# Kernel optimization log

Measured on AMD Instinct MI355X. Metric: run time of the kernel, lower is better.

The kernel has to match this reference:

```python
import jax, jax.numpy as jnp
import numpy as np

NH = 12        # main attention heads (head_dim = 64)
SNH = 4        # scorer self-attention heads
ALPHA = 0.1    # static survival-score weight
EPS = 1e-8


def _linear(x, w, b):
    # torch nn.Linear: y = x @ W^T + b
    return x @ w.T + b


def _mha(x, in_w, in_b, out_w, out_b, n_heads, maskf):
    # torch nn.MultiheadAttention (batch_first, eval mode)
    B, S, D = x.shape
    hd = D // n_heads
    qkv = _linear(x, in_w, in_b)                      # [B,S,3D]
    q, k, v = jnp.split(qkv, 3, axis=-1)
    sp = lambda t: t.reshape(B, S, n_heads, hd).transpose(0, 2, 1, 3)
    q, k, v = sp(q), sp(k), sp(v)                     # [B,h,S,hd]
    scores = jnp.einsum('bhqd,bhkd->bhqk', q, k) / jnp.asarray(np.sqrt(hd), x.dtype)
    scores = jnp.where(maskf[:, None, None, :] > 0, scores, jnp.asarray(-1e9, x.dtype))
    aw = jax.nn.softmax(scores, axis=-1)
    o = jnp.einsum('bhqk,bhkd->bhqd', aw, v).transpose(0, 2, 1, 3).reshape(B, S, D)
    return _linear(o, out_w, out_b)


def _survival_scores(x, maskf, sp_w, sp_b, sa_in_w, sa_in_b, sa_out_w, sa_out_b,
                     nw1, nb1, nw2, nb2, mw1, mb1, mw2, mb2, dw1, db1, dw2, db2):
    h = _linear(x, sp_w, sp_b)                        # [B,S,256]
    h = _mha(h, sa_in_w, sa_in_b, sa_out_w, sa_out_b, SNH, maskf)
    n = jax.nn.softplus(_linear(jax.nn.relu(_linear(h, nw1, nb1)), nw2, nb2))[..., 0]
    mu = jax.nn.sigmoid(_linear(jax.nn.relu(_linear(h, mw1, mb1)), mw2, mb2))[..., 0]
    delta = jax.nn.relu(_linear(jax.nn.relu(_linear(h, dw1, db1)), dw2, db2))[..., 0]
    # S = log(N) + log(mu / mu_c) - delta, with mu_c = 1.0
    return jnp.log(n + EPS) + jnp.log(mu + EPS) - delta


def setup_inputs() -> dict:
    key = jax.random.key(0)
    ks = iter(jax.random.split(key, 40))
    W = lambda shape: jax.random.normal(next(ks), shape, jnp.float32) * 0.05
    Z = lambda shape: jnp.zeros(shape, jnp.float32)
    B, S, H, I = 2, 2048, 768, 256
    inp = {
        'x': jax.random.normal(next(ks), (B, S, H), jnp.float32),
        'mask': jnp.ones((B, S), jnp.int32),
        'qw': W((H, H)), 'qb': Z((H,)),
        'kw': W((H, H)), 'kb': Z((H,)),
        'vw': W((H, H)), 'vb': Z((H,)),
        'ow': W((H, H)), 'ob': Z((H,)),
        'sp_w': W((I, H)), 'sp_b': Z((I,)),
        'sa_in_w': W((3 * I, I)), 'sa_in_b': Z((3 * I,)),
        'sa_out_w': W((I, I)), 'sa_out_b': Z((I,)),
        'nw1': W((I // 2, I)), 'nb1': Z((I // 2,)), 'nw2': W((1, I // 2)), 'nb2': Z((1,)),
        'mw1': W((I // 2, I)), 'mb1': Z((I // 2,)), 'mw2': W((1, I // 2)), 'mb2': Z((1,)),
        'dw1': W((I // 2, I)), 'db1': Z((I // 2,)), 'dw2': W((1, I // 2)), 'db2': Z((1,)),
    }
    return inp


def reference(x, mask, qw, qb, kw, kb, vw, vb, ow, ob,
              sp_w, sp_b, sa_in_w, sa_in_b, sa_out_w, sa_out_b,
              nw1, nb1, nw2, nb2, mw1, mb1, mw2, mb2, dw1, db1, dw2, db2):
    B, S, H = x.shape
    hd = H // NH
    maskf = mask.astype(x.dtype)
    # Q/K/V projections -> [B,h,S,hd]
    sp = lambda t: t.reshape(B, S, NH, hd).transpose(0, 2, 1, 3)
    q = sp(_linear(x, qw, qb))
    k = sp(_linear(x, kw, kb))
    v = sp(_linear(x, vw, vb))
    scores = jnp.einsum('bhqd,bhkd->bhqk', q, k) / jnp.asarray(np.sqrt(hd), x.dtype)
    # survival-score bias (broadcast over heads and query positions)
    surv = _survival_scores(x, maskf, sp_w, sp_b, sa_in_w, sa_in_b, sa_out_w, sa_out_b,
                            nw1, nb1, nw2, nb2, mw1, mb1, mw2, mb2, dw1, db1, dw2, db2)
    scores = scores + ALPHA * surv[:, None, None, :]
    scores = scores + (1.0 - maskf)[:, None, None, :] * -1e9
    aw = jax.nn.softmax(scores, axis=-1)
    out = jnp.einsum('bhqk,bhkd->bhqd', aw, v).transpose(0, 2, 1, 3).reshape(B, S, H)
    return _linear(out, ow, ob)
```

## Files before the change

### kernel.cpp

```cpp
#include <hip/hip_runtime.h>
#include <math.h>

typedef __bf16 bf16;
typedef __bf16 bfrag __attribute__((ext_vector_type(8)));
typedef __bf16 bf4 __attribute__((ext_vector_type(4)));
typedef float f4 __attribute__((ext_vector_type(4)));
typedef float f16v __attribute__((ext_vector_type(16)));

#define LOG2E 1.4426950408889634f

#define DEV static __device__ __forceinline__

DEV f4 MFMA(bfrag a, bfrag b, f4 c) {
  return __builtin_amdgcn_mfma_f32_16x16x32_bf16(a, b, c, 0, 0, 0);
}
DEV f16v MFMA32(bfrag a, bfrag b, f16v c) {
  return __builtin_amdgcn_mfma_f32_32x32x16_bf16(a, b, c, 0, 0, 0);
}
DEV float ex2(float x) { return __builtin_amdgcn_exp2f(x); }
DEV unsigned pkbf(float a, float b) {
  bf16 ha = (bf16)a, hb = (bf16)b;
  unsigned short ua = __builtin_bit_cast(unsigned short, ha);
  unsigned short ub = __builtin_bit_cast(unsigned short, hb);
  return (unsigned)ua | ((unsigned)ub << 16);
}
DEV void gload_lds16(const bf16* g, bf16* l) {
  __builtin_amdgcn_global_load_lds(
      (const __attribute__((address_space(1))) void*)g,
      (__attribute__((address_space(3))) void*)l, 16, 0, 0);
}

__global__ __launch_bounds__(256) void pack_all(
    const float* __restrict__ x, const float* __restrict__ qw, const float* __restrict__ kw,
    const float* __restrict__ vw, const float* __restrict__ ow, const float* __restrict__ sp_w,
    const float* __restrict__ sa_in_w, const float* __restrict__ sa_out_w,
    const float* __restrict__ nw1, const float* __restrict__ mw1, const float* __restrict__ dw1,
    const float* __restrict__ qb, const float* __restrict__ kb, const float* __restrict__ vb,
    const float* __restrict__ nb1, const float* __restrict__ mb1, const float* __restrict__ db1,
    const int* __restrict__ mask,
    bf16* __restrict__ xb, bf16* __restrict__ wqkv, bf16* __restrict__ wob,
    bf16* __restrict__ spwb, bf16* __restrict__ sainb, bf16* __restrict__ saoutb,
    bf16* __restrict__ w1pack, float* __restrict__ bqkv, float* __restrict__ b1pack,
    float* __restrict__ maskBias) {
  int bid = blockIdx.x;
  int tid = threadIdx.x;
  const float* src = nullptr;
  bf16* dst = nullptr;
  int rel = 0;
  if (bid < 3072)      { src = x;       dst = xb;                   rel = bid; }
  else if (bid < 3648) { src = qw;      dst = wqkv;                 rel = bid - 3072; }
  else if (bid < 4224) { src = kw;      dst = wqkv + 589824;        rel = bid - 3648; }
  else if (bid < 4800) { src = vw;      dst = wqkv + 2 * 589824;    rel = bid - 4224; }
  else if (bid < 5376) { src = ow;      dst = wob;                  rel = bid - 4800; }
  else if (bid < 5568) { src = sp_w;    dst = spwb;                 rel = bid - 5376; }
  else if (bid < 5760) { src = sa_in_w; dst = sainb;                rel = bid - 5568; }
  else if (bid < 5824) { src = sa_out_w;dst = saoutb;               rel = bid - 5760; }
  else if (bid < 5856) { src = nw1;     dst = w1pack;               rel = bid - 5824; }
  else if (bid < 5888) { src = mw1;     dst = w1pack + 32768;       rel = bid - 5856; }
  else if (bid < 5920) { src = dw1;     dst = w1pack + 2 * 32768;   rel = bid - 5888; }
  else if (bid == 5920) {
    if (tid < 576) {
      int which = tid / 192, j = tid % 192;
      const float* s = which == 0 ? qb : (which == 1 ? kb : vb);
      reinterpret_cast<float4*>(bqkv)[tid] = reinterpret_cast<const float4*>(s)[j];
    }
    return;
  } else if (bid == 5921) {
    if (tid < 96) {
      int which = tid / 32, j = tid % 32;
      const float* s = which == 0 ? nb1 : (which == 1 ? mb1 : db1);
      reinterpret_cast<float4*>(b1pack)[tid] = reinterpret_cast<const float4*>(s)[j];
    }
    return;
  } else {
    int idx = (bid - 5922) * 256 + tid;
    int4 m = reinterpret_cast<const int4*>(mask)[idx];
    float4 o;
    o.x = m.x > 0 ? 0.f : -1e9f * LOG2E;
    o.y = m.y > 0 ? 0.f : -1e9f * LOG2E;
    o.z = m.z > 0 ? 0.f : -1e9f * LOG2E;
    o.w = m.w > 0 ? 0.f : -1e9f * LOG2E;
    reinterpret_cast<float4*>(maskBias)[idx] = o;
    return;
  }
  int i = rel * 256 + tid;
  float4 v = reinterpret_cast<const float4*>(src)[i];
  bf4 o;
  o[0] = (bf16)v.x; o[1] = (bf16)v.y; o[2] = (bf16)v.z; o[3] = (bf16)v.w;
  reinterpret_cast<bf4*>(dst)[i] = o;
}

template<int OUTF32, int RELU>
__global__ __launch_bounds__(256) void gemm_nt(
    const bf16* __restrict__ A, int lda,
    const bf16* __restrict__ W, int ldw,
    const float* __restrict__ bias,
    void* __restrict__ C, int ldc,
    int N64, int K) {
  int lane = threadIdx.x & 63;
  int w = threadIdx.x >> 6;
  int lrow = lane & 15, lgrp = lane >> 4;
  int tn = blockIdx.x % N64, tm = blockIdx.x / N64;
  int m0 = tm * 64 + (w >> 1) * 32;
  int n0 = tn * 64 + (w & 1) * 32;
  const bf16* Ab = A + (size_t)m0 * lda + lgrp * 8;
  const bf16* Wb = W + (size_t)n0 * ldw + lgrp * 8;
  f4 acc[2][2] = {};
  for (int k0 = 0; k0 < K; k0 += 32) {
    bfrag a0 = *(const bfrag*)(Ab + (size_t)lrow * lda + k0);
    bfrag a1 = *(const bfrag*)(Ab + (size_t)(lrow + 16) * lda + k0);
    bfrag b0 = *(const bfrag*)(Wb + (size_t)lrow * ldw + k0);
    bfrag b1 = *(const bfrag*)(Wb + (size_t)(lrow + 16) * ldw + k0);
    acc[0][0] = MFMA(a0, b0, acc[0][0]);
    acc[0][1] = MFMA(a0, b1, acc[0][1]);
    acc[1][0] = MFMA(a1, b0, acc[1][0]);
    acc[1][1] = MFMA(a1, b1, acc[1][1]);
  }
#pragma unroll
  for (int mi = 0; mi < 2; mi++)
#pragma unroll
    for (int nj = 0; nj < 2; nj++) {
      int col = n0 + nj * 16 + lrow;
      float bv = bias[col];
      int rowb = m0 + mi * 16 + lgrp * 4;
#pragma unroll
      for (int i = 0; i < 4; i++) {
        float v = acc[mi][nj][i] + bv;
        if (RELU) v = fmaxf(v, 0.f);
        if (OUTF32)
          ((float*)C)[(size_t)(rowb + i) * ldc + col] = v;
        else
          ((bf16*)C)[(size_t)(rowb + i) * ldc + col] = (bf16)v;
      }
    }
}

template<int OUTF32>
__global__ __launch_bounds__(256, 2) void gemm_big(
    const bf16* __restrict__ A,
    const bf16* __restrict__ W,
    const float* __restrict__ bias,
    void* __restrict__ C, int ldc,
    int N128, int K) {
  __shared__ char smem[65536];
  int lane = threadIdx.x & 63;
  int w = threadIdx.x >> 6;
  int lrow = lane & 15, lgrp = lane >> 4;
  int tn = blockIdx.x % N128, tm = blockIdx.x / N128;
  int m0 = tm * 128, n0 = tn * 128;

  int srow = lane >> 3;
  int sslot = (lane & 7) ^ srow;

  auto stage = [&](int bufb, int k0) {
#pragma unroll
    for (int j = 0; j < 4; j++) {
      int rb = (w * 4 + j) * 8 + srow;
      gload_lds16(A + (size_t)(m0 + rb) * K + k0 + sslot * 8,
                  (bf16*)(smem + bufb + (w * 4 + j) * 1024));
      gload_lds16(W + (size_t)(n0 + rb) * K + k0 + sslot * 8,
                  (bf16*)(smem + bufb + 16384 + (w * 4 + j) * 1024));
    }
  };

  f4 acc[4][4] = {};
  int swz = (lrow & 7) << 4;
  int mbase = (w >> 1) * 64, nbase = (w & 1) * 64;

  stage(0, 0);
  __syncthreads();
  int buf = 0;
  int nt = K / 64;
  for (int t = 0; t < nt; t++) {
    int nbuf = buf ^ 32768;
    if (t + 1 < nt) stage(nbuf, (t + 1) * 64);
    const char* As = smem + buf;
    const char* Ws = smem + buf + 16384;
#pragma unroll
    for (int kb = 0; kb < 128; kb += 64) {
      bfrag a[4], b[4];
#pragma unroll
      for (int i = 0; i < 4; i++) {
        a[i] = *(const bfrag*)(As + (mbase + i * 16 + lrow) * 128 + ((kb + lgrp * 16) ^ swz));
        b[i] = *(const bfrag*)(Ws + (nbase + i * 16 + lrow) * 128 + ((kb + lgrp * 16) ^ swz));
      }
#pragma unroll
      for (int mi = 0; mi < 4; mi++)
#pragma unroll
        for (int nj = 0; nj < 4; nj++)
          acc[mi][nj] = MFMA(a[mi], b[nj], acc[mi][nj]);
    }
    __syncthreads();
    buf = nbuf;
  }

#pragma unroll
  for (int mi = 0; mi < 4; mi++)
#pragma unroll
    for (int nj = 0; nj < 4; nj++) {
      int col = n0 + nbase + nj * 16 + lrow;
      float bv = bias[col];
      int rowb = m0 + mbase + mi * 16 + lgrp * 4;
#pragma unroll
      for (int i = 0; i < 4; i++) {
        float v = acc[mi][nj][i] + bv;
        if (OUTF32)
          ((float*)C)[(size_t)(rowb + i) * ldc + col] = v;
        else
          ((bf16*)C)[(size_t)(rowb + i) * ldc + col] = (bf16)v;
      }
    }
}

__global__ __launch_bounds__(256) void vtrans(const bf16* __restrict__ V, int rs, int coff,
                                              bf16* __restrict__ Vt, int H, int S) {
  int nst = S / 64;
  int st = blockIdx.x % nst;
  int h = (blockIdx.x / nst) % H;
  int b = blockIdx.x / (nst * H);
  __shared__ bf16 tile[64][72];
  int t = threadIdx.x;
  int r = t >> 2, c = t & 3;
  const bf16* src = V + ((size_t)b * S + st * 64 + r) * rs + coff + h * 64 + c * 16;
  bfrag v0 = *(const bfrag*)(src);
  bfrag v1 = *(const bfrag*)(src + 8);
  *(bfrag*)&tile[r][c * 16] = v0;
  *(bfrag*)&tile[r][c * 16 + 8] = v1;
  __syncthreads();
  bf16* dst = Vt + (((size_t)b * H + h) * 64 + r) * S + st * 64 + c * 16;
  bfrag o0, o1;
#pragma unroll
  for (int j = 0; j < 8; j++) {
    o0[j] = tile[c * 16 + j][r];
    o1[j] = tile[c * 16 + 8 + j][r];
  }
  *(bfrag*)dst = o0;
  *(bfrag*)(dst + 8) = o1;
}

template<int SPLIT, int PARTIAL>
__global__ __launch_bounds__(256) void flash7_k(
    const bf16* __restrict__ Q, const bf16* __restrict__ Kp, int rs,
    const bf16* __restrict__ Vt, const float* __restrict__ bias,
    bf16* __restrict__ O, int ors,
    float* __restrict__ Opart, float* __restrict__ Lpart,
    int H, int S, float scale, int Bc) {
  int nqt = S / 128;
  int bid = blockIdx.x;
  int qt = bid % nqt;
  int hh = (bid / nqt) % H;
  int b = (bid / (nqt * H)) % Bc;
  int sp = bid / (nqt * H * Bc);
  int lane = threadIdx.x & 63, w = threadIdx.x >> 6;
  int l31 = lane & 31, hf = lane >> 5;
  int q0 = qt * 128 + w * 32;
  const int kchunk = S / SPLIT;
  int k_beg = sp * kchunk;
  int swzl = (l31 & 7) << 4;

  const bf16* Qb = Q + ((size_t)b * S + q0 + l31) * rs + hh * 64 + hf * 8;
  bfrag qf[4];
#pragma unroll
  for (int c = 0; c < 4; c++) qf[c] = *(const bfrag*)(Qb + 16 * c);

  const bf16* gK0 = Kp + ((size_t)b * S + k_beg) * rs + hh * 64;
  const bf16* gV0 = Vt + (((size_t)b * H + hh) * 64) * (size_t)S + k_beg;
  const float* biasb = bias + (size_t)b * S;

  __shared__ bf16 KT[2][4096];
  __shared__ bf16 VT[2][4096];

  f16v acc0, acc1;
#pragma unroll
  for (int r = 0; r < 16; r++) { acc0[r] = 0.f; acc1[r] = 0.f; }
  float lrun = 0.f;

  int srow = lane >> 3;
  int sel = ((lane & 7) ^ srow) * 8;
  int r0 = (w * 2) * 8 + srow;
  int r1 = (w * 2 + 1) * 8 + srow;

  auto stage = [&](int bb, int kt) {
    const bf16* gK = gK0 + (size_t)(kt - k_beg) * rs;
    const bf16* gV = gV0 + (kt - k_beg);
    gload_lds16(gK + (size_t)r0 * rs + sel, KT[bb] + (w * 2) * 512);
    gload_lds16(gK + (size_t)r1 * rs + sel, KT[bb] + (w * 2 + 1) * 512);
    gload_lds16(gV + (size_t)r0 * S + sel, VT[bb] + (w * 2) * 512);
    gload_lds16(gV + (size_t)r1 * S + sel, VT[bb] + (w * 2 + 1) * 512);
  };

  stage(0, k_beg);
  __syncthreads();

  const int nt = kchunk / 64;
  int buf = 0;
  for (int t = 0; t < nt; t++) {
    int kt = k_beg + t * 64;
    if (t + 1 < nt) stage(buf ^ 1, kt + 64);

    const char* KTb = (const char*)KT[buf];
    const char* VTb = (const char*)VT[buf];

    f16v s_lo, s_hi;
#pragma unroll
    for (int r = 0; r < 16; r++) { s_lo[r] = 0.f; s_hi[r] = 0.f; }
#pragma unroll
    for (int c = 0; c < 4; c++) {
      int colb = 32 * c + 16 * hf;
      bfrag klo = *(const bfrag*)(KTb + l31 * 128 + (colb ^ swzl));
      bfrag khi = *(const bfrag*)(KTb + (32 + l31) * 128 + (colb ^ swzl));
      s_lo = MFMA32(klo, qf[c], s_lo);
      s_hi = MFMA32(khi, qf[c], s_hi);
    }

    f4 blo[4], bhi[4];
#pragma unroll
    for (int g = 0; g < 4; g++) {
      blo[g] = *(const f4*)(biasb + kt + g * 8 + hf * 4);
      bhi[g] = *(const f4*)(biasb + kt + 32 + g * 8 + hf * 4);
    }
#pragma unroll
    for (int r = 0; r < 16; r++) {
      s_lo[r] = ex2(s_lo[r] * scale + blo[r >> 2][r & 3]);
      s_hi[r] = ex2(s_hi[r] * scale + bhi[r >> 2][r & 3]);
    }
    float rsum = s_lo[0] + s_hi[0];
#pragma unroll
    for (int r = 1; r < 16; r++) rsum += s_lo[r] + s_hi[r];
    rsum += __shfl_xor(rsum, 32);
    lrun += rsum;

    bfrag pb[4];
#pragma unroll
    for (int cc = 0; cc < 4; cc++) {
      const f16v& sv = (cc < 2) ? s_lo : s_hi;
      int rb = (cc & 1) * 8;
      unsigned lo0 = pkbf(sv[rb + 0], sv[rb + 1]);
      unsigned lo1 = pkbf(sv[rb + 2], sv[rb + 3]);
      unsigned hi0 = pkbf(sv[rb + 4], sv[rb + 5]);
      unsigned hi1 = pkbf(sv[rb + 6], sv[rb + 7]);
      unsigned t0 = hf ? lo0 : hi0;
      unsigned t1 = hf ? lo1 : hi1;
      unsigned r0s = (unsigned)__shfl_xor((int)t0, 32);
      unsigned r1s = (unsigned)__shfl_xor((int)t1, 32);
      union { bfrag v; unsigned u[4]; } pu;
      pu.u[0] = hf ? r0s : lo0;
      pu.u[1] = hf ? r1s : lo1;
      pu.u[2] = hf ? hi0 : r0s;
      pu.u[3] = hf ? hi1 : r1s;
      pb[cc] = pu.v;
    }

#pragma unroll
    for (int c = 0; c < 4; c++) {
      int colb = 32 * c + 16 * hf;
      bfrag v0 = *(const bfrag*)(VTb + l31 * 128 + (colb ^ swzl));
      bfrag v1 = *(const bfrag*)(VTb + (32 + l31) * 128 + (colb ^ swzl));
      acc0 = MFMA32(v0, pb[c], acc0);
      acc1 = MFMA32(v1, pb[c], acc1);
    }

    __syncthreads();
    buf ^= 1;
  }

  int q = q0 + l31;
  if (PARTIAL) {
    float* op = Opart + ((((size_t)sp * Bc + b) * H + hh) * S + q) * 64 + hf * 4;
#pragma unroll
    for (int g = 0; g < 4; g++) {
      f4 v0, v1;
#pragma unroll
      for (int i = 0; i < 4; i++) { v0[i] = acc0[4 * g + i]; v1[i] = acc1[4 * g + i]; }
      *(f4*)(op + g * 8) = v0;
      *(f4*)(op + 32 + g * 8) = v1;
    }
    if (hf == 0)
      Lpart[(((size_t)sp * Bc + b) * H + hh) * S + q] = lrun;
  } else {
    float inv = 1.f / lrun;
    bf16* Ob = O + ((size_t)b * S + q) * ors + hh * 64 + hf * 4;
#pragma unroll
    for (int g = 0; g < 4; g++) {
      bf4 o0, o1;
#pragma unroll
      for (int i = 0; i < 4; i++) {
        o0[i] = (bf16)(acc0[4 * g + i] * inv);
        o1[i] = (bf16)(acc1[4 * g + i] * inv);
      }
      *(bf4*)(Ob + g * 8) = o0;
      *(bf4*)(Ob + 32 + g * 8) = o1;
    }
  }
}

__global__ __launch_bounds__(256) void flash_comb(
    const float* __restrict__ Opart, const float* __restrict__ L,
    bf16* __restrict__ O, int ors, int Hh, int S, int Bc, int nsplit) {
  int idx = blockIdx.x * 256 + threadIdx.x;
  int d4 = idx & 15;
  int q = (idx >> 4) % S;
  int hh = ((idx >> 4) / S) % Hh;
  int b = (idx >> 4) / (S * Hh);
  size_t rowstride = (size_t)Bc * Hh * S;
  size_t rbase = ((size_t)b * Hh + hh) * S + q;
  float lsum = 0.f;
  f4 o = {0.f, 0.f, 0.f, 0.f};
  for (int sp = 0; sp < nsplit; sp++) {
    lsum += L[sp * rowstride + rbase];
    f4 a = *(const f4*)(Opart + (sp * rowstride + rbase) * 64 + d4 * 4);
#pragma unroll
    for (int i = 0; i < 4; i++) o[i] += a[i];
  }
  float inv = 1.f / lsum;
  bf4 obv;
#pragma unroll
  for (int i = 0; i < 4; i++) obv[i] = (bf16)(o[i] * inv);
  *(bf4*)(O + ((size_t)b * S + q) * ors + hh * 64 + d4 * 4) = obv;
}

__global__ __launch_bounds__(256) void surv_k(
    const bf16* __restrict__ hid,
    const float* __restrict__ nw2, const float* __restrict__ nb2,
    const float* __restrict__ mw2, const float* __restrict__ mb2,
    const float* __restrict__ dw2, const float* __restrict__ db2,
    const float* __restrict__ maskBias, float* __restrict__ biasMain) {
  int w = threadIdx.x >> 6, lane = threadIdx.x & 63;
  int row = blockIdx.x * 4 + w;
  const bf16* hr = hid + (size_t)row * 384;
  const float* W2[3] = {nw2, mw2, dw2};
  float outs[3];
#pragma unroll
  for (int t = 0; t < 3; t++) {
    float acc = (float)hr[t * 128 + lane] * W2[t][lane] +
                (float)hr[t * 128 + 64 + lane] * W2[t][64 + lane];
    for (int msk = 1; msk < 64; msk <<= 1) acc += __shfl_xor(acc, msk);
    outs[t] = acc;
  }
  if (lane == 0) {
    float xn = outs[0] + nb2[0];
    float n = (xn > 20.f) ? xn : log1pf(__expf(xn));
    float mu = 1.f / (1.f + __expf(-(outs[1] + mb2[0])));
    float delta = fmaxf(outs[2] + db2[0], 0.f);
    float surv = logf(n + 1e-8f) + logf(mu + 1e-8f) - delta;
    biasMain[row] = 0.1f * LOG2E * surv + maskBias[row];
  }
}

extern "C" void kernel_launch(void* const* d_in, const int* in_sizes, int n_in,
                              void* d_out, int out_size, void* d_ws, size_t ws_size,
                              hipStream_t stream) {
  const int B = 2, S = 2048, H = 768, I = 256;
  const int NH = 12, SNH = 4;
  const int M = B * S;
  const float SC = 0.125f * LOG2E;

  const float* x = (const float*)d_in[0];
  const int* mask = (const int*)d_in[1];
  const float* qw = (const float*)d_in[2];
  const float* qb = (const float*)d_in[3];
  const float* kw = (const float*)d_in[4];
  const float* kb = (const float*)d_in[5];
  const float* vw = (const float*)d_in[6];
  const float* vb = (const float*)d_in[7];
  const float* ow = (const float*)d_in[8];
  const float* ob = (const float*)d_in[9];
  const float* sp_w = (const float*)d_in[10];
  const float* sp_b = (const float*)d_in[11];
  const float* sa_in_w = (const float*)d_in[12];
  const float* sa_in_b = (const float*)d_in[13];
  const float* sa_out_w = (const float*)d_in[14];
  const float* sa_out_b = (const float*)d_in[15];
  const float* nw1 = (const float*)d_in[16];
  const float* nb1 = (const float*)d_in[17];
  const float* nw2 = (const float*)d_in[18];
  const float* nb2 = (const float*)d_in[19];
  const float* mw1 = (const float*)d_in[20];
  const float* mb1 = (const float*)d_in[21];
  const float* mw2 = (const float*)d_in[22];
  const float* mb2 = (const float*)d_in[23];
  const float* dw1 = (const float*)d_in[24];
  const float* db1 = (const float*)d_in[25];
  const float* dw2 = (const float*)d_in[26];
  const float* db2 = (const float*)d_in[27];

  char* ws = (char*)d_ws;
  size_t off = 0;
  auto alloc = [&](size_t bytes) -> void* {
    void* p = ws + off;
    off += (bytes + 255) & ~(size_t)255;
    return p;
  };

  bf16* xb = (bf16*)alloc((size_t)M * H * 2);
  bf16* wqkv = (bf16*)alloc((size_t)3 * H * H * 2);
  float* bqkv = (float*)alloc((size_t)3 * H * 4);
  bf16* wob = (bf16*)alloc((size_t)H * H * 2);
  bf16* spwb = (bf16*)alloc((size_t)I * H * 2);
  bf16* sainb = (bf16*)alloc((size_t)(3 * I) * I * 2);
  bf16* saoutb = (bf16*)alloc((size_t)I * I * 2);
  bf16* w1pack = (bf16*)alloc((size_t)384 * 256 * 2);
  float* b1pack = (float*)alloc((size_t)384 * 4);
  float* maskBias = (float*)alloc((size_t)M * 4);
  float* biasMain = (float*)alloc((size_t)M * 4);

  const int SPM = 2, SPS = 4;
  size_t offMark = off;
  bf16* h0 = (bf16*)alloc((size_t)M * I * 2);
  bf16* qkv_s = (bf16*)alloc((size_t)M * (3 * I) * 2);
  bf16* vt_s = (bf16*)alloc((size_t)B * SNH * 64 * S * 2);
  bf16* attn_s = (bf16*)alloc((size_t)M * I * 2);
  bf16* h1 = (bf16*)alloc((size_t)M * I * 2);
  bf16* hid = (bf16*)alloc((size_t)M * 384 * 2);
  float* Opart_s = (float*)alloc((size_t)SPS * B * SNH * S * 64 * 4);
  float* L_s = (float*)alloc((size_t)SPS * B * SNH * S * 4);
  size_t endA = off;
  off = offMark;
  bf16* QKVm = (bf16*)alloc((size_t)M * 3 * H * 2);
  bf16* vt_m = (bf16*)alloc((size_t)B * NH * 64 * S * 2);
  bf16* attn_m = (bf16*)alloc((size_t)M * H * 2);
  float* Opart_m = (float*)alloc((size_t)SPM * B * NH * S * 64 * 4);
  float* L_m = (float*)alloc((size_t)SPM * B * NH * S * 4);
  size_t endB = off;
  size_t need = endA > endB ? endA : endB;
  bool split_ok = ws_size >= need;
  (void)in_sizes; (void)n_in; (void)out_size;

  pack_all<<<5926, 256, 0, stream>>>(x, qw, kw, vw, ow, sp_w, sa_in_w, sa_out_w, nw1, mw1, dw1,
                                     qb, kb, vb, nb1, mb1, db1, mask,
                                     xb, wqkv, wob, spwb, sainb, saoutb, w1pack, bqkv, b1pack,
                                     maskBias);

  gemm_nt<0, 0><<<(M / 64) * (I / 64), 256, 0, stream>>>(xb, H, spwb, H, sp_b, h0, I, I / 64, H);
  gemm_nt<0, 0><<<(M / 64) * ((3 * I) / 64), 256, 0, stream>>>(h0, I, sainb, I, sa_in_b, qkv_s,
                                                               3 * I, (3 * I) / 64, I);
  vtrans<<<B * SNH * (S / 64), 256, 0, stream>>>(qkv_s, 3 * I, 2 * I, vt_s, SNH, S);
  if (split_ok) {
    flash7_k<SPS, 1><<<SPS * B * SNH * (S / 128), 256, 0, stream>>>(
        qkv_s, qkv_s + I, 3 * I, vt_s, maskBias, nullptr, 0, Opart_s, L_s, SNH, S, SC, B);
    flash_comb<<<(B * SNH * S * 16) / 256, 256, 0, stream>>>(Opart_s, L_s, attn_s, I, SNH, S,
                                                             B, SPS);
  } else {
    flash7_k<1, 0><<<B * SNH * (S / 128), 256, 0, stream>>>(
        qkv_s, qkv_s + I, 3 * I, vt_s, maskBias, attn_s, I, nullptr, nullptr, SNH, S, SC, B);
  }
  gemm_nt<0, 0><<<(M / 64) * (I / 64), 256, 0, stream>>>(attn_s, I, saoutb, I, sa_out_b, h1, I,
                                                         I / 64, I);
  gemm_nt<0, 1><<<(M / 64) * (384 / 64), 256, 0, stream>>>(h1, I, w1pack, I, b1pack, hid, 384,
                                                           384 / 64, I);
  surv_k<<<M / 4, 256, 0, stream>>>(hid, nw2, nb2, mw2, mb2, dw2, db2, maskBias, biasMain);

  gemm_big<0><<<(M / 128) * (3 * H / 128), 256, 0, stream>>>(xb, wqkv, bqkv, QKVm, 3 * H,
                                                             3 * H / 128, H);
  vtrans<<<B * NH * (S / 64), 256, 0, stream>>>(QKVm, 3 * H, 2 * H, vt_m, NH, S);
  if (split_ok) {
    flash7_k<SPM, 1><<<SPM * B * NH * (S / 128), 256, 0, stream>>>(
        QKVm, QKVm + H, 3 * H, vt_m, biasMain, nullptr, 0, Opart_m, L_m, NH, S, SC, B);
    flash_comb<<<(B * NH * S * 16) / 256, 256, 0, stream>>>(Opart_m, L_m, attn_m, H, NH, S, B,
                                                            SPM);
  } else {
    flash7_k<1, 0><<<B * NH * (S / 128), 256, 0, stream>>>(
        QKVm, QKVm + H, 3 * H, vt_m, biasMain, attn_m, H, nullptr, nullptr, NH, S, SC, B);
  }
  gemm_big<1><<<(M / 128) * (H / 128), 256, 0, stream>>>(attn_m, wob, ob, d_out, H,
                                                         H / 128, H);
}
```

Measured before the change: 196.8 us.

## Split KV range across warp pairs inside block and merge in LDS

The flash attention kernel now uses 64-query tiles, with the block's two warp pairs each processing half of the KV chunk. Their partial accumulators and row sums are merged through shared memory, which replaces a cross-block split plus combine kernel for the main attention and halves the scorer split. It also uses v_cvt_pk_bf16_f32 and permlane32_swap for the P fragment repack, and adds s_setprio around the MFMA sections. The cost is 64KB of LDS per block, which may limit occupancy, plus an extra barrier and exchange at the end.

After: 197.5 us. About the same (+0.4%).

```diff
diff --git a/kernel.cpp b/kernel.cpp
--- a/kernel.cpp
+++ b/kernel.cpp
@@ -6,6 +6,7 @@
 typedef __bf16 bf4 __attribute__((ext_vector_type(4)));
 typedef float f4 __attribute__((ext_vector_type(4)));
 typedef float f16v __attribute__((ext_vector_type(16)));
+typedef unsigned uint2v __attribute__((ext_vector_type(2)));
 
 #define LOG2E 1.4426950408889634f
 
@@ -18,11 +19,8 @@
   return __builtin_amdgcn_mfma_f32_32x32x16_bf16(a, b, c, 0, 0, 0);
 }
 DEV float ex2(float x) { return __builtin_amdgcn_exp2f(x); }
-DEV unsigned pkbf(float a, float b) {
-  bf16 ha = (bf16)a, hb = (bf16)b;
-  unsigned short ua = __builtin_bit_cast(unsigned short, ha);
-  unsigned short ub = __builtin_bit_cast(unsigned short, hb);
-  return (unsigned)ua | ((unsigned)ub << 16);
+DEV uint2v pl32(unsigned a, unsigned b) {
+  return __builtin_amdgcn_permlane32_swap(a, b, false, false);
 }
 DEV void gload_lds16(const bf16* g, bf16* l) {
   __builtin_amdgcn_global_load_lds(
@@ -239,23 +237,26 @@
 }
 
 template<int SPLIT, int PARTIAL>
-__global__ __launch_bounds__(256) void flash7_k(
+__global__ __launch_bounds__(256) void flash8_k(
     const bf16* __restrict__ Q, const bf16* __restrict__ Kp, int rs,
     const bf16* __restrict__ Vt, const float* __restrict__ bias,
     bf16* __restrict__ O, int ors,
     float* __restrict__ Opart, float* __restrict__ Lpart,
     int H, int S, float scale, int Bc) {
-  int nqt = S / 128;
+  __shared__ char smem[65536];
+  int nqt = S / 64;
   int bid = blockIdx.x;
   int qt = bid % nqt;
   int hh = (bid / nqt) % H;
   int b = (bid / (nqt * H)) % Bc;
   int sp = bid / (nqt * H * Bc);
   int lane = threadIdx.x & 63, w = threadIdx.x >> 6;
+  int wi = w & 1, half = w >> 1;
   int l31 = lane & 31, hf = lane >> 5;
-  int q0 = qt * 128 + w * 32;
+  int q0 = qt * 64 + wi * 32;
   const int kchunk = S / SPLIT;
-  int k_beg = sp * kchunk;
+  const int khalf = kchunk / 2;
+  int k_beg = sp * kchunk + half * khalf;
   int swzl = (l31 & 7) << 4;
 
   const bf16* Qb = Q + ((size_t)b * S + q0 + l31) * rs + hh * 64 + hf * 8;
@@ -267,9 +268,6 @@
   const bf16* gV0 = Vt + (((size_t)b * H + hh) * 64) * (size_t)S + k_beg;
   const float* biasb = bias + (size_t)b * S;
 
-  __shared__ bf16 KT[2][4096];
-  __shared__ bf16 VT[2][4096];
-
   f16v acc0, acc1;
 #pragma unroll
   for (int r = 0; r < 16; r++) { acc0[r] = 0.f; acc1[r] = 0.f; }
@@ -277,33 +275,35 @@
 
   int srow = lane >> 3;
   int sel = ((lane & 7) ^ srow) * 8;
-  int r0 = (w * 2) * 8 + srow;
-  int r1 = (w * 2 + 1) * 8 + srow;
-
-  auto stage = [&](int bb, int kt) {
-    const bf16* gK = gK0 + (size_t)(kt - k_beg) * rs;
-    const bf16* gV = gV0 + (kt - k_beg);
-    gload_lds16(gK + (size_t)r0 * rs + sel, KT[bb] + (w * 2) * 512);
-    gload_lds16(gK + (size_t)r1 * rs + sel, KT[bb] + (w * 2 + 1) * 512);
-    gload_lds16(gV + (size_t)r0 * S + sel, VT[bb] + (w * 2) * 512);
-    gload_lds16(gV + (size_t)r1 * S + sel, VT[bb] + (w * 2 + 1) * 512);
+
+  auto stage = [&](int bb, int trel) {
+    const bf16* gK = gK0 + (size_t)trel * 64 * rs;
+    const bf16* gV = gV0 + trel * 64;
+    char* base = smem + (half * 2 + bb) * 16384;
+#pragma unroll
+    for (int j = 0; j < 4; j++) {
+      int r = wi * 32 + j * 8 + srow;
+      gload_lds16(gK + (size_t)r * rs + sel, (bf16*)(base + (wi * 32 + j * 8) * 128));
+      gload_lds16(gV + (size_t)r * S + sel, (bf16*)(base + 8192 + (wi * 32 + j * 8) * 128));
+    }
   };
 
-  stage(0, k_beg);
+  stage(0, 0);
   __syncthreads();
 
-  const int nt = kchunk / 64;
+  const int nt = khalf / 64;
   int buf = 0;
   for (int t = 0; t < nt; t++) {
     int kt = k_beg + t * 64;
-    if (t + 1 < nt) stage(buf ^ 1, kt + 64);
-
-    const char* KTb = (const char*)KT[buf];
-    const char* VTb = (const char*)VT[buf];
+    if (t + 1 < nt) stage(buf ^ 1, t + 1);
+
+    const char* KTb = smem + (half * 2 + buf) * 16384;
+    const char* VTb = KTb + 8192;
 
     f16v s_lo, s_hi;
 #pragma unroll
     for (int r = 0; r < 16; r++) { s_lo[r] = 0.f; s_hi[r] = 0.f; }
+    __builtin_amdgcn_s_setprio(1);
 #pragma unroll
     for (int c = 0; c < 4; c++) {
       int colb = 32 * c + 16 * hf;
@@ -312,6 +312,7 @@
       s_lo = MFMA32(klo, qf[c], s_lo);
       s_hi = MFMA32(khi, qf[c], s_hi);
     }
+    __builtin_amdgcn_s_setprio(0);
 
     f4 blo[4], bhi[4];
 #pragma unroll
@@ -335,22 +336,19 @@
     for (int cc = 0; cc < 4; cc++) {
       const f16v& sv = (cc < 2) ? s_lo : s_hi;
       int rb = (cc & 1) * 8;
-      unsigned lo0 = pkbf(sv[rb + 0], sv[rb + 1]);
-      unsigned lo1 = pkbf(sv[rb + 2], sv[rb + 3]);
-      unsigned hi0 = pkbf(sv[rb + 4], sv[rb + 5]);
-      unsigned hi1 = pkbf(sv[rb + 6], sv[rb + 7]);
-      unsigned t0 = hf ? lo0 : hi0;
-      unsigned t1 = hf ? lo1 : hi1;
-      unsigned r0s = (unsigned)__shfl_xor((int)t0, 32);
-      unsigned r1s = (unsigned)__shfl_xor((int)t1, 32);
+      unsigned lo0, lo1, hi0, hi1;
+      asm("v_cvt_pk_bf16_f32 %0, %1, %2" : "=v"(lo0) : "v"(sv[rb + 0]), "v"(sv[rb + 1]));
+      asm("v_cvt_pk_bf16_f32 %0, %1, %2" : "=v"(lo1) : "v"(sv[rb + 2]), "v"(sv[rb + 3]));
+      asm("v_cvt_pk_bf16_f32 %0, %1, %2" : "=v"(hi0) : "v"(sv[rb + 4]), "v"(sv[rb + 5]));
+      asm("v_cvt_pk_bf16_f32 %0, %1, %2" : "=v"(hi1) : "v"(sv[rb + 6]), "v"(sv[rb + 7]));
+      uint2v e0 = pl32(lo0, hi0);
+      uint2v e1 = pl32(lo1, hi1);
       union { bfrag v; unsigned u[4]; } pu;
-      pu.u[0] = hf ? r0s : lo0;
-      pu.u[1] = hf ? r1s : lo1;
-      pu.u[2] = hf ? hi0 : r0s;
-      pu.u[3] = hf ? hi1 : r1s;
+      pu.u[0] = e0[0]; pu.u[1] = e1[0]; pu.u[2] = e0[1]; pu.u[3] = e1[1];
       pb[cc] = pu.v;
     }
 
+    __builtin_amdgcn_s_setprio(1);
 #pragma unroll
     for (int c = 0; c < 4; c++) {
       int colb = 32 * c + 16 * hf;
@@ -359,37 +357,64 @@
       acc0 = MFMA32(v0, pb[c], acc0);
       acc1 = MFMA32(v1, pb[c], acc1);
     }
+    __builtin_amdgcn_s_setprio(0);
 
     __syncthreads();
     buf ^= 1;
   }
 
-  int q = q0 + l31;
-  if (PARTIAL) {
-    float* op = Opart + ((((size_t)sp * Bc + b) * H + hh) * S + q) * 64 + hf * 4;
-#pragma unroll
-    for (int g = 0; g < 4; g++) {
-      f4 v0, v1;
-#pragma unroll
-      for (int i = 0; i < 4; i++) { v0[i] = acc0[4 * g + i]; v1[i] = acc1[4 * g + i]; }
-      *(f4*)(op + g * 8) = v0;
-      *(f4*)(op + 32 + g * 8) = v1;
-    }
-    if (hf == 0)
-      Lpart[(((size_t)sp * Bc + b) * H + hh) * S + q] = lrun;
-  } else {
-    float inv = 1.f / lrun;
-    bf16* Ob = O + ((size_t)b * S + q) * ors + hh * 64 + hf * 4;
-#pragma unroll
-    for (int g = 0; g < 4; g++) {
-      bf4 o0, o1;
+  float* exch = (float*)smem;
+  float* exl = (float*)(smem + 32768);
+  if (half == 1) {
+#pragma unroll
+    for (int g = 0; g < 8; g++) {
+      f4 v;
+#pragma unroll
+      for (int i = 0; i < 4; i++) v[i] = (g < 4) ? acc0[g * 4 + i] : acc1[(g - 4) * 4 + i];
+      *(f4*)(exch + ((size_t)wi * 8 + g) * 256 + lane * 4) = v;
+    }
+    exl[wi * 64 + lane] = lrun;
+  }
+  __syncthreads();
+  if (half == 0) {
+#pragma unroll
+    for (int g = 0; g < 8; g++) {
+      f4 v = *(const f4*)(exch + ((size_t)wi * 8 + g) * 256 + lane * 4);
 #pragma unroll
       for (int i = 0; i < 4; i++) {
-        o0[i] = (bf16)(acc0[4 * g + i] * inv);
-        o1[i] = (bf16)(acc1[4 * g + i] * inv);
+        if (g < 4) acc0[g * 4 + i] += v[i];
+        else       acc1[(g - 4) * 4 + i] += v[i];
       }
-      *(bf4*)(Ob + g * 8) = o0;
-      *(bf4*)(Ob + 32 + g * 8) = o1;
+    }
+    lrun += exl[wi * 64 + lane];
+
+    int q = q0 + l31;
+    if (PARTIAL) {
+      float* op = Opart + ((((size_t)sp * Bc + b) * H + hh) * S + q) * 64 + hf * 4;
+#pragma unroll
+      for (int g = 0; g < 4; g++) {
+        f4 v0, v1;
+#pragma unroll
+        for (int i = 0; i < 4; i++) { v0[i] = acc0[4 * g + i]; v1[i] = acc1[4 * g + i]; }
+        *(f4*)(op + g * 8) = v0;
+        *(f4*)(op + 32 + g * 8) = v1;
+      }
+      if (hf == 0)
+        Lpart[(((size_t)sp * Bc + b) * H + hh) * S + q] = lrun;
+    } else {
+      float inv = 1.f / lrun;
+      bf16* Ob = O + ((size_t)b * S + q) * ors + hh * 64 + hf * 4;
+#pragma unroll
+      for (int g = 0; g < 4; g++) {
+        bf4 o0, o1;
+#pragma unroll
+        for (int i = 0; i < 4; i++) {
+          o0[i] = (bf16)(acc0[4 * g + i] * inv);
+          o1[i] = (bf16)(acc1[4 * g + i] * inv);
+        }
+        *(bf4*)(Ob + g * 8) = o0;
+        *(bf4*)(Ob + 32 + g * 8) = o1;
+      }
     }
   }
 }
@@ -504,7 +529,7 @@
   float* maskBias = (float*)alloc((size_t)M * 4);
   float* biasMain = (float*)alloc((size_t)M * 4);
 
-  const int SPM = 2, SPS = 4;
+  const int SPS = 2;
   size_t offMark = off;
   bf16* h0 = (bf16*)alloc((size_t)M * I * 2);
   bf16* qkv_s = (bf16*)alloc((size_t)M * (3 * I) * 2);
@@ -519,8 +544,6 @@
   bf16* QKVm = (bf16*)alloc((size_t)M * 3 * H * 2);
   bf16* vt_m = (bf16*)alloc((size_t)B * NH * 64 * S * 2);
   bf16* attn_m = (bf16*)alloc((size_t)M * H * 2);
-  float* Opart_m = (float*)alloc((size_t)SPM * B * NH * S * 64 * 4);
-  float* L_m = (float*)alloc((size_t)SPM * B * NH * S * 4);
   size_t endB = off;
   size_t need = endA > endB ? endA : endB;
   bool split_ok = ws_size >= need;
@@ -536,12 +559,12 @@
                                                                3 * I, (3 * I) / 64, I);
   vtrans<<<B * SNH * (S / 64), 256, 0, stream>>>(qkv_s, 3 * I, 2 * I, vt_s, SNH, S);
   if (split_ok) {
-    flash7_k<SPS, 1><<<SPS * B * SNH * (S / 128), 256, 0, stream>>>(
+    flash8_k<SPS, 1><<<SPS * B * SNH * (S / 64), 256, 0, stream>>>(
         qkv_s, qkv_s + I, 3 * I, vt_s, maskBias, nullptr, 0, Opart_s, L_s, SNH, S, SC, B);
     flash_comb<<<(B * SNH * S * 16) / 256, 256, 0, stream>>>(Opart_s, L_s, attn_s, I, SNH, S,
                                                              B, SPS);
   } else {
-    flash7_k<1, 0><<<B * SNH * (S / 128), 256, 0, stream>>>(
+    flash8_k<1, 0><<<B * SNH * (S / 64), 256, 0, stream>>>(
         qkv_s, qkv_s + I, 3 * I, vt_s, maskBias, attn_s, I, nullptr, nullptr, SNH, S, SC, B);
   }
   gemm_nt<0, 0><<<(M / 64) * (I / 64), 256, 0, stream>>>(attn_s, I, saoutb, I, sa_out_b, h1, I,
@@ -553,15 +576,8 @@
   gemm_big<0><<<(M / 128) * (3 * H / 128), 256, 0, stream>>>(xb, wqkv, bqkv, QKVm, 3 * H,
                                                              3 * H / 128, H);
   vtrans<<<B * NH * (S / 64), 256, 0, stream>>>(QKVm, 3 * H, 2 * H, vt_m, NH, S);
-  if (split_ok) {
-    flash7_k<SPM, 1><<<SPM * B * NH * (S / 128), 256, 0, stream>>>(
-        QKVm, QKVm + H, 3 * H, vt_m, biasMain, nullptr, 0, Opart_m, L_m, NH, S, SC, B);
-    flash_comb<<<(B * NH * S * 16) / 256, 256, 0, stream>>>(Opart_m, L_m, attn_m, H, NH, S, B,
-                                                            SPM);
-  } else {
-    flash7_k<1, 0><<<B * NH * (S / 128), 256, 0, stream>>>(
-        QKVm, QKVm + H, 3 * H, vt_m, biasMain, attn_m, H, nullptr, nullptr, NH, S, SC, B);
-  }
+  flash8_k<1, 0><<<B * NH * (S / 64), 256, 0, stream>>>(
+      QKVm, QKVm + H, 3 * H, vt_m, biasMain, attn_m, H, nullptr, nullptr, NH, S, SC, B);
   gemm_big<1><<<(M / 128) * (H / 128), 256, 0, stream>>>(attn_m, wob, ob, d_out, H,
                                                          H / 128, H);
 }
```

## Fuse scorer projection into main QKV GEMM and tune flash softmax packing

Applied to the files above, without the earlier changes.

The scorer input projection (sp_w) and the main Q/K/V projections both read x, so their weights are concatenated into one 2560-wide matrix and computed by a single large GEMM. Downstream kernels then read slices of that fused output. This removes one kernel launch and a second pass over x. In the flash kernel, bf16 packing now uses v_cvt_pk_bf16_f32 with permlane32_swap in place of shuffles, and wave priority is raised around the MFMA blocks. The fused output buffer sits outside the aliased workspace region, which raises workspace use, and the main QKV result now has to be produced before the scorer path rather than overlapping it.

After: 176.1 us. 1.12x faster.

```diff
diff --git a/kernel.cpp b/kernel.cpp
--- a/kernel.cpp
+++ b/kernel.cpp
@@ -6,6 +6,7 @@
 typedef __bf16 bf4 __attribute__((ext_vector_type(4)));
 typedef float f4 __attribute__((ext_vector_type(4)));
 typedef float f16v __attribute__((ext_vector_type(16)));
+typedef unsigned uint2v __attribute__((ext_vector_type(2)));
 
 #define LOG2E 1.4426950408889634f
 
@@ -18,11 +19,8 @@
   return __builtin_amdgcn_mfma_f32_32x32x16_bf16(a, b, c, 0, 0, 0);
 }
 DEV float ex2(float x) { return __builtin_amdgcn_exp2f(x); }
-DEV unsigned pkbf(float a, float b) {
-  bf16 ha = (bf16)a, hb = (bf16)b;
-  unsigned short ua = __builtin_bit_cast(unsigned short, ha);
-  unsigned short ub = __builtin_bit_cast(unsigned short, hb);
-  return (unsigned)ua | ((unsigned)ub << 16);
+DEV uint2v pl32(unsigned a, unsigned b) {
+  return __builtin_amdgcn_permlane32_swap(a, b, false, false);
 }
 DEV void gload_lds16(const bf16* g, bf16* l) {
   __builtin_amdgcn_global_load_lds(
@@ -35,12 +33,13 @@
     const float* __restrict__ vw, const float* __restrict__ ow, const float* __restrict__ sp_w,
     const float* __restrict__ sa_in_w, const float* __restrict__ sa_out_w,
     const float* __restrict__ nw1, const float* __restrict__ mw1, const float* __restrict__ dw1,
-    const float* __restrict__ qb, const float* __restrict__ kb, const float* __restrict__ vb,
+    const float* __restrict__ sp_b, const float* __restrict__ qb, const float* __restrict__ kb,
+    const float* __restrict__ vb,
     const float* __restrict__ nb1, const float* __restrict__ mb1, const float* __restrict__ db1,
     const int* __restrict__ mask,
-    bf16* __restrict__ xb, bf16* __restrict__ wqkv, bf16* __restrict__ wob,
-    bf16* __restrict__ spwb, bf16* __restrict__ sainb, bf16* __restrict__ saoutb,
-    bf16* __restrict__ w1pack, float* __restrict__ bqkv, float* __restrict__ b1pack,
+    bf16* __restrict__ xb, bf16* __restrict__ wfused, bf16* __restrict__ wob,
+    bf16* __restrict__ sainb, bf16* __restrict__ saoutb,
+    bf16* __restrict__ w1pack, float* __restrict__ bfused, float* __restrict__ b1pack,
     float* __restrict__ maskBias) {
   int bid = blockIdx.x;
   int tid = threadIdx.x;
@@ -48,21 +47,25 @@
   bf16* dst = nullptr;
   int rel = 0;
   if (bid < 3072)      { src = x;       dst = xb;                   rel = bid; }
-  else if (bid < 3648) { src = qw;      dst = wqkv;                 rel = bid - 3072; }
-  else if (bid < 4224) { src = kw;      dst = wqkv + 589824;        rel = bid - 3648; }
-  else if (bid < 4800) { src = vw;      dst = wqkv + 2 * 589824;    rel = bid - 4224; }
-  else if (bid < 5376) { src = ow;      dst = wob;                  rel = bid - 4800; }
-  else if (bid < 5568) { src = sp_w;    dst = spwb;                 rel = bid - 5376; }
+  else if (bid < 3264) { src = sp_w;    dst = wfused;               rel = bid - 3072; }
+  else if (bid < 3840) { src = qw;      dst = wfused + 196608;      rel = bid - 3264; }
+  else if (bid < 4416) { src = kw;      dst = wfused + 786432;      rel = bid - 3840; }
+  else if (bid < 4992) { src = vw;      dst = wfused + 1376256;     rel = bid - 4416; }
+  else if (bid < 5568) { src = ow;      dst = wob;                  rel = bid - 4992; }
   else if (bid < 5760) { src = sa_in_w; dst = sainb;                rel = bid - 5568; }
   else if (bid < 5824) { src = sa_out_w;dst = saoutb;               rel = bid - 5760; }
   else if (bid < 5856) { src = nw1;     dst = w1pack;               rel = bid - 5824; }
   else if (bid < 5888) { src = mw1;     dst = w1pack + 32768;       rel = bid - 5856; }
   else if (bid < 5920) { src = dw1;     dst = w1pack + 2 * 32768;   rel = bid - 5888; }
   else if (bid == 5920) {
-    if (tid < 576) {
-      int which = tid / 192, j = tid % 192;
-      const float* s = which == 0 ? qb : (which == 1 ? kb : vb);
-      reinterpret_cast<float4*>(bqkv)[tid] = reinterpret_cast<const float4*>(s)[j];
+    for (int t = tid; t < 640; t += 256) {
+      const float* s;
+      int j;
+      if (t < 64)       { s = sp_b; j = t; }
+      else if (t < 256) { s = qb;   j = t - 64; }
+      else if (t < 448) { s = kb;   j = t - 256; }
+      else              { s = vb;   j = t - 448; }
+      reinterpret_cast<float4*>(bfused)[t] = reinterpret_cast<const float4*>(s)[j];
     }
     return;
   } else if (bid == 5921) {
@@ -239,7 +242,7 @@
 }
 
 template<int SPLIT, int PARTIAL>
-__global__ __launch_bounds__(256) void flash7_k(
+__global__ __launch_bounds__(256) void flash9_k(
     const bf16* __restrict__ Q, const bf16* __restrict__ Kp, int rs,
     const bf16* __restrict__ Vt, const float* __restrict__ bias,
     bf16* __restrict__ O, int ors,
@@ -280,23 +283,23 @@
   int r0 = (w * 2) * 8 + srow;
   int r1 = (w * 2 + 1) * 8 + srow;
 
-  auto stage = [&](int bb, int kt) {
-    const bf16* gK = gK0 + (size_t)(kt - k_beg) * rs;
-    const bf16* gV = gV0 + (kt - k_beg);
+  auto stage = [&](int bb, int trel) {
+    const bf16* gK = gK0 + (size_t)trel * 64 * rs;
+    const bf16* gV = gV0 + trel * 64;
     gload_lds16(gK + (size_t)r0 * rs + sel, KT[bb] + (w * 2) * 512);
     gload_lds16(gK + (size_t)r1 * rs + sel, KT[bb] + (w * 2 + 1) * 512);
     gload_lds16(gV + (size_t)r0 * S + sel, VT[bb] + (w * 2) * 512);
     gload_lds16(gV + (size_t)r1 * S + sel, VT[bb] + (w * 2 + 1) * 512);
   };
 
-  stage(0, k_beg);
+  stage(0, 0);
   __syncthreads();
 
   const int nt = kchunk / 64;
   int buf = 0;
   for (int t = 0; t < nt; t++) {
     int kt = k_beg + t * 64;
-    if (t + 1 < nt) stage(buf ^ 1, kt + 64);
+    if (t + 1 < nt) stage(buf ^ 1, t + 1);
 
     const char* KTb = (const char*)KT[buf];
     const char* VTb = (const char*)VT[buf];
@@ -304,6 +307,7 @@
     f16v s_lo, s_hi;
 #pragma unroll
     for (int r = 0; r < 16; r++) { s_lo[r] = 0.f; s_hi[r] = 0.f; }
+    __builtin_amdgcn_s_setprio(1);
 #pragma unroll
     for (int c = 0; c < 4; c++) {
       int colb = 32 * c + 16 * hf;
@@ -312,6 +316,7 @@
       s_lo = MFMA32(klo, qf[c], s_lo);
       s_hi = MFMA32(khi, qf[c], s_hi);
     }
+    __builtin_amdgcn_s_setprio(0);
 
     f4 blo[4], bhi[4];
 #pragma unroll
@@ -335,22 +340,19 @@
     for (int cc = 0; cc < 4; cc++) {
       const f16v& sv = (cc < 2) ? s_lo : s_hi;
       int rb = (cc & 1) * 8;
-      unsigned lo0 = pkbf(sv[rb + 0], sv[rb + 1]);
-      unsigned lo1 = pkbf(sv[rb + 2], sv[rb + 3]);
-      unsigned hi0 = pkbf(sv[rb + 4], sv[rb + 5]);
-      unsigned hi1 = pkbf(sv[rb + 6], sv[rb + 7]);
-      unsigned t0 = hf ? lo0 : hi0;
-      unsigned t1 = hf ? lo1 : hi1;
-      unsigned r0s = (unsigned)__shfl_xor((int)t0, 32);
-      unsigned r1s = (unsigned)__shfl_xor((int)t1, 32);
+      unsigned lo0, lo1, hi0, hi1;
+      asm("v_cvt_pk_bf16_f32 %0, %1, %2" : "=v"(lo0) : "v"(sv[rb + 0]), "v"(sv[rb + 1]));
+      asm("v_cvt_pk_bf16_f32 %0, %1, %2" : "=v"(lo1) : "v"(sv[rb + 2]), "v"(sv[rb + 3]));
+      asm("v_cvt_pk_bf16_f32 %0, %1, %2" : "=v"(hi0) : "v"(sv[rb + 4]), "v"(sv[rb + 5]));
+      asm("v_cvt_pk_bf16_f32 %0, %1, %2" : "=v"(hi1) : "v"(sv[rb + 6]), "v"(sv[rb + 7]));
+      uint2v e0 = pl32(lo0, hi0);
+      uint2v e1 = pl32(lo1, hi1);
       union { bfrag v; unsigned u[4]; } pu;
-      pu.u[0] = hf ? r0s : lo0;
-      pu.u[1] = hf ? r1s : lo1;
-      pu.u[2] = hf ? hi0 : r0s;
-      pu.u[3] = hf ? hi1 : r1s;
+      pu.u[0] = e0[0]; pu.u[1] = e1[0]; pu.u[2] = e0[1]; pu.u[3] = e1[1];
       pb[cc] = pu.v;
     }
 
+    __builtin_amdgcn_s_setprio(1);
 #pragma unroll
     for (int c = 0; c < 4; c++) {
       int colb = 32 * c + 16 * hf;
@@ -359,6 +361,7 @@
       acc0 = MFMA32(v0, pb[c], acc0);
       acc1 = MFMA32(v1, pb[c], acc1);
     }
+    __builtin_amdgcn_s_setprio(0);
 
     __syncthreads();
     buf ^= 1;
@@ -453,6 +456,7 @@
   const int B = 2, S = 2048, H = 768, I = 256;
   const int NH = 12, SNH = 4;
   const int M = B * S;
+  const int NF = 2560;
   const float SC = 0.125f * LOG2E;
 
   const float* x = (const float*)d_in[0];
@@ -493,20 +497,19 @@
   };
 
   bf16* xb = (bf16*)alloc((size_t)M * H * 2);
-  bf16* wqkv = (bf16*)alloc((size_t)3 * H * H * 2);
-  float* bqkv = (float*)alloc((size_t)3 * H * 4);
+  bf16* wfused = (bf16*)alloc((size_t)NF * H * 2);
+  float* bfused = (float*)alloc((size_t)NF * 4);
   bf16* wob = (bf16*)alloc((size_t)H * H * 2);
-  bf16* spwb = (bf16*)alloc((size_t)I * H * 2);
   bf16* sainb = (bf16*)alloc((size_t)(3 * I) * I * 2);
   bf16* saoutb = (bf16*)alloc((size_t)I * I * 2);
   bf16* w1pack = (bf16*)alloc((size_t)384 * 256 * 2);
   float* b1pack = (float*)alloc((size_t)384 * 4);
   float* maskBias = (float*)alloc((size_t)M * 4);
   float* biasMain = (float*)alloc((size_t)M * 4);
+  bf16* Cfused = (bf16*)alloc((size_t)M * NF * 2);
 
   const int SPM = 2, SPS = 4;
   size_t offMark = off;
-  bf16* h0 = (bf16*)alloc((size_t)M * I * 2);
   bf16* qkv_s = (bf16*)alloc((size_t)M * (3 * I) * 2);
   bf16* vt_s = (bf16*)alloc((size_t)B * SNH * 64 * S * 2);
   bf16* attn_s = (bf16*)alloc((size_t)M * I * 2);
@@ -516,7 +519,6 @@
   float* L_s = (float*)alloc((size_t)SPS * B * SNH * S * 4);
   size_t endA = off;
   off = offMark;
-  bf16* QKVm = (bf16*)alloc((size_t)M * 3 * H * 2);
   bf16* vt_m = (bf16*)alloc((size_t)B * NH * 64 * S * 2);
   bf16* attn_m = (bf16*)alloc((size_t)M * H * 2);
   float* Opart_m = (float*)alloc((size_t)SPM * B * NH * S * 64 * 4);
@@ -527,21 +529,23 @@
   (void)in_sizes; (void)n_in; (void)out_size;
 
   pack_all<<<5926, 256, 0, stream>>>(x, qw, kw, vw, ow, sp_w, sa_in_w, sa_out_w, nw1, mw1, dw1,
-                                     qb, kb, vb, nb1, mb1, db1, mask,
-                                     xb, wqkv, wob, spwb, sainb, saoutb, w1pack, bqkv, b1pack,
+                                     sp_b, qb, kb, vb, nb1, mb1, db1, mask,
+                                     xb, wfused, wob, sainb, saoutb, w1pack, bfused, b1pack,
                                      maskBias);
 
-  gemm_nt<0, 0><<<(M / 64) * (I / 64), 256, 0, stream>>>(xb, H, spwb, H, sp_b, h0, I, I / 64, H);
-  gemm_nt<0, 0><<<(M / 64) * ((3 * I) / 64), 256, 0, stream>>>(h0, I, sainb, I, sa_in_b, qkv_s,
-                                                               3 * I, (3 * I) / 64, I);
+  gemm_big<0><<<(M / 128) * (NF / 128), 256, 0, stream>>>(xb, wfused, bfused, Cfused, NF,
+                                                          NF / 128, H);
+
+  gemm_nt<0, 0><<<(M / 64) * ((3 * I) / 64), 256, 0, stream>>>(Cfused, NF, sainb, I, sa_in_b,
+                                                               qkv_s, 3 * I, (3 * I) / 64, I);
   vtrans<<<B * SNH * (S / 64), 256, 0, stream>>>(qkv_s, 3 * I, 2 * I, vt_s, SNH, S);
   if (split_ok) {
-    flash7_k<SPS, 1><<<SPS * B * SNH * (S / 128), 256, 0, stream>>>(
+    flash9_k<SPS, 1><<<SPS * B * SNH * (S / 128), 256, 0, stream>>>(
         qkv_s, qkv_s + I, 3 * I, vt_s, maskBias, nullptr, 0, Opart_s, L_s, SNH, S, SC, B);
     flash_comb<<<(B * SNH * S * 16) / 256, 256, 0, stream>>>(Opart_s, L_s, attn_s, I, SNH, S,
                                                              B, SPS);
   } else {
-    flash7_k<1, 0><<<B * SNH * (S / 128), 256, 0, stream>>>(
+    flash9_k<1, 0><<<B * SNH * (S / 128), 256, 0, stream>>>(
         qkv_s, qkv_s + I, 3 * I, vt_s, maskBias, attn_s, I, nullptr, nullptr, SNH, S, SC, B);
   }
   gemm_nt<0, 0><<<(M / 64) * (I / 64), 256, 0, stream>>>(attn_s, I, saoutb, I, sa_out_b, h1, I,
@@ -550,17 +554,17 @@
                                                            384 / 64, I);
   surv_k<<<M / 4, 256, 0, stream>>>(hid, nw2, nb2, mw2, mb2, dw2, db2, maskBias, biasMain);
 
-  gemm_big<0><<<(M / 128) * (3 * H / 128), 256, 0, stream>>>(xb, wqkv, bqkv, QKVm, 3 * H,
-                                                             3 * H / 128, H);
-  vtrans<<<B * NH * (S / 64), 256, 0, stream>>>(QKVm, 3 * H, 2 * H, vt_m, NH, S);
+  vtrans<<<B * NH * (S / 64), 256, 0, stream>>>(Cfused, NF, 1792, vt_m, NH, S);
   if (split_ok) {
-    flash7_k<SPM, 1><<<SPM * B * NH * (S / 128), 256, 0, stream>>>(
-        QKVm, QKVm + H, 3 * H, vt_m, biasMain, nullptr, 0, Opart_m, L_m, NH, S, SC, B);
+    flash9_k<SPM, 1><<<SPM * B * NH * (S / 128), 256, 0, stream>>>(
+        Cfused + 256, Cfused + 1024, NF, vt_m, biasMain, nullptr, 0, Opart_m, L_m, NH, S, SC,
+        B);
     flash_comb<<<(B * NH * S * 16) / 256, 256, 0, stream>>>(Opart_m, L_m, attn_m, H, NH, S, B,
                                                             SPM);
   } else {
-    flash7_k<1, 0><<<B * NH * (S / 128), 256, 0, stream>>>(
-        QKVm, QKVm + H, 3 * H, vt_m, biasMain, attn_m, H, nullptr, nullptr, NH, S, SC, B);
+    flash9_k<1, 0><<<B * NH * (S / 128), 256, 0, stream>>>(
+        Cfused + 256, Cfused + 1024, NF, vt_m, biasMain, attn_m, H, nullptr, nullptr, NH, S,
+        SC, B);
   }
   gemm_big<1><<<(M / 128) * (H / 128), 256, 0, stream>>>(attn_m, wob, ob, d_out, H,
                                                          H / 128, H);
```
